# Optimization experiments

Measured on AMD Instinct MI355X. Metric: run time of the kernel, lower is better.

## Reference

```python
import jax, jax.numpy as jnp
import numpy as np

B, N, DIM, T, H, DH = 4, 2048, 512, 16, 8, 64
EPS = 1e-5


def setup_inputs() -> dict:
    key = jax.random.key(0)
    ks = jax.random.split(key, 7)
    x = jax.random.normal(ks[0], (B, N, DIM), dtype=jnp.float32)
    # time-distance matrix, e.g. months between scans, in [0, 24)
    R = jax.random.uniform(ks[1], (B, T, T), dtype=jnp.float32) * 24.0
    gamma = jnp.ones((DIM,), dtype=jnp.float32)
    beta = jnp.zeros((DIM,), dtype=jnp.float32)
    W_qkv = jax.random.normal(ks[2], (DIM, 3 * H * DH), dtype=jnp.float32) * 0.02
    W_out = jax.random.normal(ks[3], (H * DH, DIM), dtype=jnp.float32) * 0.02
    a = jax.random.uniform(ks[4], (H,), dtype=jnp.float32)          # torch.rand(heads)
    c = 12.0 * jax.random.uniform(ks[5], (H,), dtype=jnp.float32)   # 12 * torch.rand(heads)
    return {"x": x, "R": R, "gamma": gamma, "beta": beta,
            "W_qkv": W_qkv, "W_out": W_out, "a": a, "c": c}


def reference(x, R, gamma, beta, W_qkv, W_out, a, c):
    b, n, dim = x.shape
    t = R.shape[-1]
    num_patches = n // t
    scale = DH ** -0.5

    # LayerNorm
    mu = jnp.mean(x, axis=-1, keepdims=True)
    var = jnp.mean(jnp.square(x - mu), axis=-1, keepdims=True)
    xn = (x - mu) * jax.lax.rsqrt(var + EPS) * gamma + beta

    # QKV projection -> [b, h, n, d]
    qkv = xn @ W_qkv  # [b, n, 3*h*d]
    q, k, v = jnp.split(qkv, 3, axis=-1)
    def to_heads(z):
        return z.reshape(b, n, H, DH).transpose(0, 2, 1, 3)
    q, k, v = to_heads(q), to_heads(k), to_heads(v)

    # attention scores with ReLU then learned sigmoid time-decay mask
    dots = jnp.einsum('bhnd,bhmd->bhnm', q, k) * scale
    dots = jax.nn.relu(dots)

    # flipped-sigmoid decay: 1 / (1 + exp(|a|*R - |c|)), per head  -> [b, h, t, t]
    decay = 1.0 / (1.0 + jnp.exp(jnp.abs(a)[None, :, None, None] * R[:, None, :, :]
                                 - jnp.abs(c)[None, :, None, None]))
    # expand timepoint mask to token resolution (repeat_interleave on both axes)
    decay = jnp.repeat(jnp.repeat(decay, num_patches, axis=2), num_patches, axis=3)

    attn = jax.nn.softmax(dots * decay, axis=-1)
    out = jnp.einsum('bhnm,bhmd->bhnd', attn, v)
    out = out.transpose(0, 2, 1, 3).reshape(b, n, H * DH)
    return out @ W_out  # dropout is identity at eval
```

## Files before the change

### kernel.cpp

```cpp
#include <hip/hip_runtime.h>
#include <math.h>

#define B_   4
#define N_   2048
#define DIM_ 512
#define T_   16
#define H_   8
#define DH_  64

typedef unsigned short ushort_t;
typedef __attribute__((ext_vector_type(8))) short bf16x8;
typedef __attribute__((ext_vector_type(16))) float f32x16;

__device__ inline ushort_t bf16_rn(float x) {
  unsigned u = __builtin_bit_cast(unsigned, x);
  u += 0x7FFFu + ((u >> 16) & 1u);
  return (ushort_t)(u >> 16);
}
__device__ inline float bf16f(ushort_t h) {
  return __builtin_bit_cast(float, (unsigned)h << 16);
}
__device__ inline unsigned pack2(ushort_t a, ushort_t b) {
  return (unsigned)a | ((unsigned)b << 16);
}
__device__ inline void split2(float x, ushort_t &h, ushort_t &l) {
  h = bf16_rn(x);
  l = bf16_rn(x - bf16f(h));
}

__global__ __launch_bounds__(256) void transpose_split_kernel(
    const float* __restrict__ src, ushort_t* __restrict__ dh,
    ushort_t* __restrict__ dl, int K, int Nn) {
  __shared__ float Ts[64][68];
  int tid = threadIdx.x;
  int n0 = blockIdx.x * 64;
  int k0 = blockIdx.y * 64;
#pragma unroll
  for (int it = 0; it < 4; ++it) {
    int idx = tid + it * 256;
    int r = idx >> 4, c4 = (idx & 15) * 4;
    *(float4*)&Ts[r][c4] = *(const float4*)&src[(size_t)(k0 + r) * Nn + n0 + c4];
  }
  __syncthreads();
#pragma unroll
  for (int it = 0; it < 2; ++it) {
    int idx = tid + it * 256;
    int n = idx >> 3, kc = (idx & 7) * 8;
    ushort_t hs[8], ls[8];
#pragma unroll
    for (int j = 0; j < 8; ++j) split2(Ts[kc + j][n], hs[j], ls[j]);
    uint4 uh, ul;
    uh.x = pack2(hs[0], hs[1]); uh.y = pack2(hs[2], hs[3]);
    uh.z = pack2(hs[4], hs[5]); uh.w = pack2(hs[6], hs[7]);
    ul.x = pack2(ls[0], ls[1]); ul.y = pack2(ls[2], ls[3]);
    ul.z = pack2(ls[4], ls[5]); ul.w = pack2(ls[6], ls[7]);
    size_t o = (size_t)(n0 + n) * K + k0 + kc;
    *(uint4*)&dh[o] = uh;
    *(uint4*)&dl[o] = ul;
  }
}

__global__ __launch_bounds__(256) void ln_xn_kernel(
    const float* __restrict__ x, const float* __restrict__ gamma,
    const float* __restrict__ beta, ushort_t* __restrict__ xnh,
    ushort_t* __restrict__ xnl) {
  int row  = blockIdx.x * 4 + (threadIdx.x >> 6);
  int lane = threadIdx.x & 63;
  const float4* xr = (const float4*)(x + (size_t)row * DIM_);
  float4 v0 = xr[lane * 2 + 0];
  float4 v1 = xr[lane * 2 + 1];
  float s  = v0.x + v0.y + v0.z + v0.w + v1.x + v1.y + v1.z + v1.w;
  float ss = v0.x*v0.x + v0.y*v0.y + v0.z*v0.z + v0.w*v0.w
           + v1.x*v1.x + v1.y*v1.y + v1.z*v1.z + v1.w*v1.w;
#pragma unroll
  for (int off = 32; off > 0; off >>= 1) {
    s  += __shfl_xor(s, off);
    ss += __shfl_xor(ss, off);
  }
  float mu  = s * (1.0f / DIM_);
  float var = ss * (1.0f / DIM_) - mu * mu;
  float rstd = rsqrtf(var + 1e-5f);
  float4 g0 = *(const float4*)&gamma[lane * 8];
  float4 g1 = *(const float4*)&gamma[lane * 8 + 4];
  float4 b0 = *(const float4*)&beta[lane * 8];
  float4 b1 = *(const float4*)&beta[lane * 8 + 4];
  float xv[8] = {v0.x, v0.y, v0.z, v0.w, v1.x, v1.y, v1.z, v1.w};
  float gv[8] = {g0.x, g0.y, g0.z, g0.w, g1.x, g1.y, g1.z, g1.w};
  float bv[8] = {b0.x, b0.y, b0.z, b0.w, b1.x, b1.y, b1.z, b1.w};
  ushort_t hs[8], ls[8];
#pragma unroll
  for (int j = 0; j < 8; ++j) {
    float xn = (xv[j] - mu) * rstd * gv[j] + bv[j];
    split2(xn, hs[j], ls[j]);
  }
  uint4 uh, ul;
  uh.x = pack2(hs[0], hs[1]); uh.y = pack2(hs[2], hs[3]);
  uh.z = pack2(hs[4], hs[5]); uh.w = pack2(hs[6], hs[7]);
  ul.x = pack2(ls[0], ls[1]); ul.y = pack2(ls[2], ls[3]);
  ul.z = pack2(ls[4], ls[5]); ul.w = pack2(ls[6], ls[7]);
  size_t o = (size_t)row * DIM_ + lane * 8;
  *(uint4*)&xnh[o] = uh;
  *(uint4*)&xnl[o] = ul;
}

__global__ __launch_bounds__(256) void qkv_gemm_mfma(
    const ushort_t* __restrict__ xnh, const ushort_t* __restrict__ xnl,
    const ushort_t* __restrict__ wth, const ushort_t* __restrict__ wtl,
    ushort_t* __restrict__ qh, ushort_t* __restrict__ ql,
    ushort_t* __restrict__ kho, ushort_t* __restrict__ klo,
    ushort_t* __restrict__ vt) {
  __shared__ ushort_t Ah[128 * 40], Al[128 * 40], Bh[128 * 40], Bl[128 * 40];
  int tid = threadIdx.x;
  int w = tid >> 6, lane = tid & 63, l31 = lane & 31, g = lane >> 5;
  int wm = w >> 1, wn = w & 1;
  int n0 = blockIdx.x * 128;
  int m0 = blockIdx.y * 128;

  f32x16 acc[2][2];
#pragma unroll
  for (int i = 0; i < 2; ++i)
#pragma unroll
    for (int j = 0; j < 2; ++j)
#pragma unroll
      for (int e = 0; e < 16; ++e) acc[i][j][e] = 0.0f;

  int fm[2], fc[2];
#pragma unroll
  for (int it = 0; it < 2; ++it) {
    int f = tid + it * 256;
    fm[it] = f >> 2;
    fc[it] = (f & 3) * 8;
  }

#pragma unroll 1
  for (int kt = 0; kt < 16; ++kt) {
    __syncthreads();
#pragma unroll
    for (int it = 0; it < 2; ++it) {
      size_t ao = (size_t)(m0 + fm[it]) * 512 + kt * 32 + fc[it];
      size_t bo = (size_t)(n0 + fm[it]) * 512 + kt * 32 + fc[it];
      uint4 tah = *(const uint4*)&xnh[ao];
      uint4 tal = *(const uint4*)&xnl[ao];
      uint4 tbh = *(const uint4*)&wth[bo];
      uint4 tbl = *(const uint4*)&wtl[bo];
      int o = fm[it] * 40 + fc[it];
      *(uint4*)&Ah[o] = tah;
      *(uint4*)&Al[o] = tal;
      *(uint4*)&Bh[o] = tbh;
      *(uint4*)&Bl[o] = tbl;
    }
    __syncthreads();
#pragma unroll
    for (int kc = 0; kc < 2; ++kc) {
      int off = kc * 16 + 8 * g;
      bf16x8 afh[2], afl[2], bfh[2], bfl[2];
#pragma unroll
      for (int rb = 0; rb < 2; ++rb) {
        int r = (wm * 64 + rb * 32 + l31) * 40 + off;
        afh[rb] = *(const bf16x8*)&Ah[r];
        afl[rb] = *(const bf16x8*)&Al[r];
      }
#pragma unroll
      for (int cb = 0; cb < 2; ++cb) {
        int r = (wn * 64 + cb * 32 + l31) * 40 + off;
        bfh[cb] = *(const bf16x8*)&Bh[r];
        bfl[cb] = *(const bf16x8*)&Bl[r];
      }
#pragma unroll
      for (int rb = 0; rb < 2; ++rb)
#pragma unroll
        for (int cb = 0; cb < 2; ++cb) {
          acc[rb][cb] = __builtin_amdgcn_mfma_f32_32x32x16_bf16(afh[rb], bfh[cb], acc[rb][cb], 0, 0, 0);
          acc[rb][cb] = __builtin_amdgcn_mfma_f32_32x32x16_bf16(afh[rb], bfl[cb], acc[rb][cb], 0, 0, 0);
          acc[rb][cb] = __builtin_amdgcn_mfma_f32_32x32x16_bf16(afl[rb], bfh[cb], acc[rb][cb], 0, 0, 0);
        }
    }
  }

  int part = n0 >> 9;
#pragma unroll
  for (int rb = 0; rb < 2; ++rb) {
    int m_base = m0 + wm * 64 + rb * 32;
#pragma unroll
    for (int cb = 0; cb < 2; ++cb) {
      int n_g = n0 + wn * 64 + cb * 32 + l31;
      int rem = n_g & 511, hh = rem >> 6, d = rem & 63;
      if (part == 2) {
#pragma unroll
        for (int grp = 0; grp < 4; ++grp) {
          int m_g = m_base + grp * 8 + 4 * g;
          int bb = m_g >> 11, tok = m_g & 2047;
          uint2 pk;
          pk.x = pack2(bf16_rn(acc[rb][cb][grp * 4 + 0]), bf16_rn(acc[rb][cb][grp * 4 + 1]));
          pk.y = pack2(bf16_rn(acc[rb][cb][grp * 4 + 2]), bf16_rn(acc[rb][cb][grp * 4 + 3]));
          *(uint2*)&vt[((size_t)(bb * 8 + hh) * 64 + d) * 2048 + tok] = pk;
        }
      } else {
        float sc = (part == 0) ? 0.125f : 1.0f;
        ushort_t* dsth = (part == 0) ? qh : kho;
        ushort_t* dstl = (part == 0) ? ql : klo;
#pragma unroll
        for (int reg = 0; reg < 16; ++reg) {
          int row = (reg & 3) + 8 * (reg >> 2) + 4 * g;
          int m_g = m_base + row;
          int bb = m_g >> 11, tok = m_g & 2047;
          ushort_t hi, lo;
          split2(acc[rb][cb][reg] * sc, hi, lo);
          size_t addr = ((size_t)(bb * 8 + hh) * 2048 + tok) * 64 + d;
          dsth[addr] = hi;
          dstl[addr] = lo;
        }
      }
    }
  }
}

__global__ __launch_bounds__(256) void attn_mfma(
    const ushort_t* __restrict__ qh, const ushort_t* __restrict__ ql,
    const ushort_t* __restrict__ kho, const ushort_t* __restrict__ klo,
    const ushort_t* __restrict__ vt, const float* __restrict__ R,
    const float* __restrict__ a, const float* __restrict__ c,
    ushort_t* __restrict__ aoh, ushort_t* __restrict__ aol) {
  __shared__ ushort_t KhS[64 * 72], KlS[64 * 72], VtS[64 * 72], PS[64 * 72];
  __shared__ float rsLDS[2][64];

  int tid = threadIdx.x;
  int w = tid >> 6, lane = tid & 63, l31 = lane & 31, g = lane >> 5;
  int qhalf = w >> 1, khalf = w & 1;
  int bh = blockIdx.x;
  int qt = blockIdx.y;
  int b = bh >> 3, h = bh & 7;
  float aab = fabsf(a[h]);
  float cab = fabsf(c[h]);

  size_t qoff = ((size_t)bh * 2048 + qt * 64 + qhalf * 32 + l31) * 64;
  bf16x8 qfh[4], qfl[4];
#pragma unroll
  for (int d0i = 0; d0i < 4; ++d0i) {
    qfh[d0i] = *(const bf16x8*)&qh[qoff + d0i * 16 + 8 * g];
    qfl[d0i] = *(const bf16x8*)&ql[qoff + d0i * 16 + 8 * g];
  }

  int frow[2], fcc[2];
#pragma unroll
  for (int it = 0; it < 2; ++it) {
    int f = tid + it * 256;
    frow[it] = f >> 3;
    fcc[it] = (f & 7) * 8;
  }
  const ushort_t* kbase = kho + (size_t)bh * 2048 * 64;
  const ushort_t* lbase = klo + (size_t)bh * 2048 * 64;
  const ushort_t* vbase = vt + (size_t)bh * 64 * 2048;

  f32x16 oacc;
#pragma unroll
  for (int i = 0; i < 16; ++i) oacc[i] = 0.0f;
  float rs_acc[16] = {};
  int ti = qt >> 1;

#pragma unroll 1
  for (int kt = 0; kt < 32; ++kt) {
    __syncthreads();
#pragma unroll
    for (int it = 0; it < 2; ++it) {
      uint4 tk = *(const uint4*)&kbase[(size_t)(kt * 64 + frow[it]) * 64 + fcc[it]];
      uint4 tl = *(const uint4*)&lbase[(size_t)(kt * 64 + frow[it]) * 64 + fcc[it]];
      uint4 tv = *(const uint4*)&vbase[(size_t)frow[it] * 2048 + kt * 64 + fcc[it]];
      int o = frow[it] * 72 + fcc[it];
      *(uint4*)&KhS[o] = tk;
      *(uint4*)&KlS[o] = tl;
      *(uint4*)&VtS[o] = tv;
    }
    __syncthreads();

    f32x16 sacc;
#pragma unroll
    for (int i = 0; i < 16; ++i) sacc[i] = 0.0f;
    int krow = (khalf * 32 + l31) * 72;
#pragma unroll
    for (int d0i = 0; d0i < 4; ++d0i) {
      int off = krow + d0i * 16 + 8 * g;
      bf16x8 kfh = *(const bf16x8*)&KhS[off];
      bf16x8 kfl = *(const bf16x8*)&KlS[off];
      sacc = __builtin_amdgcn_mfma_f32_32x32x16_bf16(qfh[d0i], kfh, sacc, 0, 0, 0);
      sacc = __builtin_amdgcn_mfma_f32_32x32x16_bf16(qfh[d0i], kfl, sacc, 0, 0, 0);
      sacc = __builtin_amdgcn_mfma_f32_32x32x16_bf16(qfl[d0i], kfh, sacc, 0, 0, 0);
    }

    float Rv = R[b * (T_ * T_) + ti * T_ + (kt >> 1)];
    float dec = 1.0f / (1.0f + __expf(aab * Rv - cab));
#pragma unroll
    for (int reg = 0; reg < 16; ++reg) {
      float pv = __expf(fmaxf(sacc[reg], 0.0f) * dec);
      rs_acc[reg] += pv;
      int row = (reg & 3) + 8 * (reg >> 2) + 4 * g;
      PS[(qhalf * 32 + row) * 72 + khalf * 32 + l31] = bf16_rn(pv);
    }
    __syncthreads();

#pragma unroll
    for (int k0i = 0; k0i < 4; ++k0i) {
      bf16x8 pf = *(const bf16x8*)&PS[(qhalf * 32 + l31) * 72 + k0i * 16 + 8 * g];
      bf16x8 vf = *(const bf16x8*)&VtS[(khalf * 32 + l31) * 72 + k0i * 16 + 8 * g];
      oacc = __builtin_amdgcn_mfma_f32_32x32x16_bf16(pf, vf, oacc, 0, 0, 0);
    }
  }

#pragma unroll
  for (int reg = 0; reg < 16; ++reg) {
    float vsum = rs_acc[reg];
    vsum += __shfl_xor(vsum, 1);
    vsum += __shfl_xor(vsum, 2);
    vsum += __shfl_xor(vsum, 4);
    vsum += __shfl_xor(vsum, 8);
    vsum += __shfl_xor(vsum, 16);
    rs_acc[reg] = vsum;
  }
  if (l31 == 0) {
#pragma unroll
    for (int reg = 0; reg < 16; ++reg) {
      int row = (reg & 3) + 8 * (reg >> 2) + 4 * g;
      rsLDS[khalf][qhalf * 32 + row] = rs_acc[reg];
    }
  }
  __syncthreads();

#pragma unroll
  for (int reg = 0; reg < 16; ++reg) {
    int row = (reg & 3) + 8 * (reg >> 2) + 4 * g;
    int qg = qhalf * 32 + row;
    float invs = 1.0f / (rsLDS[0][qg] + rsLDS[1][qg]);
    int tok = qt * 64 + qg;
    int d = khalf * 32 + l31;
    ushort_t hi, lo;
    split2(oacc[reg] * invs, hi, lo);
    size_t addr = ((size_t)b * 2048 + tok) * 512 + h * 64 + d;
    aoh[addr] = hi;
    aol[addr] = lo;
  }
}

__global__ __launch_bounds__(256) void out_gemm_mfma(
    const ushort_t* __restrict__ ah, const ushort_t* __restrict__ al,
    const ushort_t* __restrict__ wth, const ushort_t* __restrict__ wtl,
    float* __restrict__ out) {
  __shared__ ushort_t Ah[128 * 40], Al[128 * 40], Bh[128 * 40], Bl[128 * 40];
  int tid = threadIdx.x;
  int w = tid >> 6, lane = tid & 63, l31 = lane & 31, g = lane >> 5;
  int wm = w >> 1, wn = w & 1;
  int n0 = blockIdx.x * 128;
  int m0 = blockIdx.y * 128;

  f32x16 acc[2][2];
#pragma unroll
  for (int i = 0; i < 2; ++i)
#pragma unroll
    for (int j = 0; j < 2; ++j)
#pragma unroll
      for (int e = 0; e < 16; ++e) acc[i][j][e] = 0.0f;

  int fm[2], fc[2];
#pragma unroll
  for (int it = 0; it < 2; ++it) {
    int f = tid + it * 256;
    fm[it] = f >> 2;
    fc[it] = (f & 3) * 8;
  }

#pragma unroll 1
  for (int kt = 0; kt < 16; ++kt) {
    __syncthreads();
#pragma unroll
    for (int it = 0; it < 2; ++it) {
      size_t ao = (size_t)(m0 + fm[it]) * 512 + kt * 32 + fc[it];
      size_t bo = (size_t)(n0 + fm[it]) * 512 + kt * 32 + fc[it];
      uint4 tah = *(const uint4*)&ah[ao];
      uint4 tal = *(const uint4*)&al[ao];
      uint4 tbh = *(const uint4*)&wth[bo];
      uint4 tbl = *(const uint4*)&wtl[bo];
      int o = fm[it] * 40 + fc[it];
      *(uint4*)&Ah[o] = tah;
      *(uint4*)&Al[o] = tal;
      *(uint4*)&Bh[o] = tbh;
      *(uint4*)&Bl[o] = tbl;
    }
    __syncthreads();
#pragma unroll
    for (int kc = 0; kc < 2; ++kc) {
      int off = kc * 16 + 8 * g;
      bf16x8 afh[2], afl[2], bfh[2], bfl[2];
#pragma unroll
      for (int rb = 0; rb < 2; ++rb) {
        int r = (wm * 64 + rb * 32 + l31) * 40 + off;
        afh[rb] = *(const bf16x8*)&Ah[r];
        afl[rb] = *(const bf16x8*)&Al[r];
      }
#pragma unroll
      for (int cb = 0; cb < 2; ++cb) {
        int r = (wn * 64 + cb * 32 + l31) * 40 + off;
        bfh[cb] = *(const bf16x8*)&Bh[r];
        bfl[cb] = *(const bf16x8*)&Bl[r];
      }
#pragma unroll
      for (int rb = 0; rb < 2; ++rb)
#pragma unroll
        for (int cb = 0; cb < 2; ++cb) {
          acc[rb][cb] = __builtin_amdgcn_mfma_f32_32x32x16_bf16(afh[rb], bfh[cb], acc[rb][cb], 0, 0, 0);
          acc[rb][cb] = __builtin_amdgcn_mfma_f32_32x32x16_bf16(afh[rb], bfl[cb], acc[rb][cb], 0, 0, 0);
          acc[rb][cb] = __builtin_amdgcn_mfma_f32_32x32x16_bf16(afl[rb], bfh[cb], acc[rb][cb], 0, 0, 0);
        }
    }
  }

#pragma unroll
  for (int rb = 0; rb < 2; ++rb) {
    int m_base = m0 + wm * 64 + rb * 32;
#pragma unroll
    for (int cb = 0; cb < 2; ++cb) {
      int n_g = n0 + wn * 64 + cb * 32 + l31;
#pragma unroll
      for (int reg = 0; reg < 16; ++reg) {
        int row = (reg & 3) + 8 * (reg >> 2) + 4 * g;
        out[(size_t)(m_base + row) * 512 + n_g] = acc[rb][cb][reg];
      }
    }
  }
}

extern "C" void kernel_launch(void* const* d_in, const int* in_sizes, int n_in,
                              void* d_out, int out_size, void* d_ws, size_t ws_size,
                              hipStream_t stream) {
  (void)in_sizes; (void)n_in;
  const float* x     = (const float*)d_in[0];
  const float* R     = (const float*)d_in[1];
  const float* gamma = (const float*)d_in[2];
  const float* beta  = (const float*)d_in[3];
  const float* Wqkv  = (const float*)d_in[4];
  const float* Wout  = (const float*)d_in[5];
  const float* av    = (const float*)d_in[6];
  const float* cv    = (const float*)d_in[7];
  float* out = (float*)d_out;

  const size_t EL  = (size_t)B_ * N_ * DIM_;
  const size_t SZT = EL * sizeof(ushort_t);

  char* p = (char*)d_ws;
  ushort_t* wqh = (ushort_t*)p;                  p += (size_t)1536 * 512 * 2;
  ushort_t* wql = (ushort_t*)p;                  p += (size_t)1536 * 512 * 2;
  ushort_t* woh = (ushort_t*)p;                  p += (size_t)512 * 512 * 2;
  ushort_t* wol = (ushort_t*)p;                  p += (size_t)512 * 512 * 2;
  ushort_t* qhb = (ushort_t*)p;                  p += SZT;
  ushort_t* qlb = (ushort_t*)p;                  p += SZT;
  ushort_t* khb = (ushort_t*)p;                  p += SZT;
  ushort_t* klb = (ushort_t*)p;                  p += SZT;
  ushort_t* vtb = (ushort_t*)p;                  p += SZT;
  size_t base_need = (size_t)(p - (char*)d_ws);
  size_t needA = base_need + 2 * SZT;

  bool planA = (ws_size >= needA);
  ushort_t* xnh = planA ? (ushort_t*)p : (ushort_t*)d_out;
  ushort_t* xnl = xnh + EL;
  float* gemm_dst = planA ? out : (float*)qhb;

  transpose_split_kernel<<<dim3(24, 8), dim3(256), 0, stream>>>(Wqkv, wqh, wql, 512, 1536);
  transpose_split_kernel<<<dim3(8, 8), dim3(256), 0, stream>>>(Wout, woh, wol, 512, 512);
  ln_xn_kernel<<<dim3(2048), dim3(256), 0, stream>>>(x, gamma, beta, xnh, xnl);
  qkv_gemm_mfma<<<dim3(12, 64), dim3(256), 0, stream>>>(xnh, xnl, wqh, wql,
                                                        qhb, qlb, khb, klb, vtb);
  attn_mfma<<<dim3(32, 32), dim3(256), 0, stream>>>(qhb, qlb, khb, klb, vtb,
                                                    R, av, cv, xnh, xnl);
  out_gemm_mfma<<<dim3(4, 64), dim3(256), 0, stream>>>(xnh, xnl, woh, wol, gemm_dst);
  if (!planA) {
    hipMemcpyAsync(out, gemm_dst, (size_t)out_size * sizeof(float),
                   hipMemcpyDeviceToDevice, stream);
  }
}
```

Baseline: 263.7 us.

## Merge prep kernels, add XCD-aware GEMM block mapping, use exp2 softmax

Merges the two weight transpose/split launches and the LayerNorm launch into one prep kernel that dispatches on block index, which saves launch overhead and lets the three jobs overlap. The QKV and output GEMMs switch to a 1D grid with a block-to-tile mapping that keeps the M tiles handled by the same XCD together, aiming for better L2 reuse on the MI355X's chiplets. In attention, the log2(e) factor is folded into the decay so exp2f replaces __expf, and bf16 conversion of P uses round-half-up in place of round-to-nearest-even. That rounding change alters numerics slightly.

```diff
diff --git a/kernel.cpp b/kernel.cpp
--- a/kernel.cpp
+++ b/kernel.cpp
@@ -28,79 +28,88 @@
   l = bf16_rn(x - bf16f(h));
 }
 
-__global__ __launch_bounds__(256) void transpose_split_kernel(
-    const float* __restrict__ src, ushort_t* __restrict__ dh,
-    ushort_t* __restrict__ dl, int K, int Nn) {
+__global__ __launch_bounds__(256) void prep_kernel(
+    const float* __restrict__ x, const float* __restrict__ gamma,
+    const float* __restrict__ beta, const float* __restrict__ Wqkv,
+    const float* __restrict__ Wout,
+    ushort_t* __restrict__ xnh, ushort_t* __restrict__ xnl,
+    ushort_t* __restrict__ wqh, ushort_t* __restrict__ wql,
+    ushort_t* __restrict__ woh, ushort_t* __restrict__ wol) {
   __shared__ float Ts[64][68];
+  int bidx = blockIdx.x;
   int tid = threadIdx.x;
-  int n0 = blockIdx.x * 64;
-  int k0 = blockIdx.y * 64;
-#pragma unroll
-  for (int it = 0; it < 4; ++it) {
-    int idx = tid + it * 256;
-    int r = idx >> 4, c4 = (idx & 15) * 4;
-    *(float4*)&Ts[r][c4] = *(const float4*)&src[(size_t)(k0 + r) * Nn + n0 + c4];
-  }
-  __syncthreads();
-#pragma unroll
-  for (int it = 0; it < 2; ++it) {
-    int idx = tid + it * 256;
-    int n = idx >> 3, kc = (idx & 7) * 8;
+  if (bidx < 256) {
+    const float* src; ushort_t* dh; ushort_t* dl; int Nn, n0, k0;
+    if (bidx < 192) {
+      src = Wqkv; dh = wqh; dl = wql; Nn = 1536;
+      n0 = (bidx % 24) * 64; k0 = (bidx / 24) * 64;
+    } else {
+      int l = bidx - 192;
+      src = Wout; dh = woh; dl = wol; Nn = 512;
+      n0 = (l % 8) * 64; k0 = (l / 8) * 64;
+    }
+#pragma unroll
+    for (int it = 0; it < 4; ++it) {
+      int idx = tid + it * 256;
+      int r = idx >> 4, c4 = (idx & 15) * 4;
+      *(float4*)&Ts[r][c4] = *(const float4*)&src[(size_t)(k0 + r) * Nn + n0 + c4];
+    }
+    __syncthreads();
+#pragma unroll
+    for (int it = 0; it < 2; ++it) {
+      int idx = tid + it * 256;
+      int n = idx >> 3, kc = (idx & 7) * 8;
+      ushort_t hs[8], ls[8];
+#pragma unroll
+      for (int j = 0; j < 8; ++j) split2(Ts[kc + j][n], hs[j], ls[j]);
+      uint4 uh, ul;
+      uh.x = pack2(hs[0], hs[1]); uh.y = pack2(hs[2], hs[3]);
+      uh.z = pack2(hs[4], hs[5]); uh.w = pack2(hs[6], hs[7]);
+      ul.x = pack2(ls[0], ls[1]); ul.y = pack2(ls[2], ls[3]);
+      ul.z = pack2(ls[4], ls[5]); ul.w = pack2(ls[6], ls[7]);
+      size_t o = (size_t)(n0 + n) * 512 + k0 + kc;
+      *(uint4*)&dh[o] = uh;
+      *(uint4*)&dl[o] = ul;
+    }
+  } else {
+    int row  = (bidx - 256) * 4 + (tid >> 6);
+    int lane = tid & 63;
+    const float4* xr = (const float4*)(x + (size_t)row * DIM_);
+    float4 v0 = xr[lane * 2 + 0];
+    float4 v1 = xr[lane * 2 + 1];
+    float s  = v0.x + v0.y + v0.z + v0.w + v1.x + v1.y + v1.z + v1.w;
+    float ss = v0.x*v0.x + v0.y*v0.y + v0.z*v0.z + v0.w*v0.w
+             + v1.x*v1.x + v1.y*v1.y + v1.z*v1.z + v1.w*v1.w;
+#pragma unroll
+    for (int off = 32; off > 0; off >>= 1) {
+      s  += __shfl_xor(s, off);
+      ss += __shfl_xor(ss, off);
+    }
+    float mu  = s * (1.0f / DIM_);
+    float var = ss * (1.0f / DIM_) - mu * mu;
+    float rstd = rsqrtf(var + 1e-5f);
+    float4 g0 = *(const float4*)&gamma[lane * 8];
+    float4 g1 = *(const float4*)&gamma[lane * 8 + 4];
+    float4 b0 = *(const float4*)&beta[lane * 8];
+    float4 b1 = *(const float4*)&beta[lane * 8 + 4];
+    float xv[8] = {v0.x, v0.y, v0.z, v0.w, v1.x, v1.y, v1.z, v1.w};
+    float gv[8] = {g0.x, g0.y, g0.z, g0.w, g1.x, g1.y, g1.z, g1.w};
+    float bv[8] = {b0.x, b0.y, b0.z, b0.w, b1.x, b1.y, b1.z, b1.w};
     ushort_t hs[8], ls[8];
 #pragma unroll
-    for (int j = 0; j < 8; ++j) split2(Ts[kc + j][n], hs[j], ls[j]);
+    for (int j = 0; j < 8; ++j) {
+      float xn = (xv[j] - mu) * rstd * gv[j] + bv[j];
+      split2(xn, hs[j], ls[j]);
+    }
     uint4 uh, ul;
     uh.x = pack2(hs[0], hs[1]); uh.y = pack2(hs[2], hs[3]);
     uh.z = pack2(hs[4], hs[5]); uh.w = pack2(hs[6], hs[7]);
     ul.x = pack2(ls[0], ls[1]); ul.y = pack2(ls[2], ls[3]);
     ul.z = pack2(ls[4], ls[5]); ul.w = pack2(ls[6], ls[7]);
-    size_t o = (size_t)(n0 + n) * K + k0 + kc;
-    *(uint4*)&dh[o] = uh;
-    *(uint4*)&dl[o] = ul;
-  }
-}
-
-__global__ __launch_bounds__(256) void ln_xn_kernel(
-    const float* __restrict__ x, const float* __restrict__ gamma,
-    const float* __restrict__ beta, ushort_t* __restrict__ xnh,
-    ushort_t* __restrict__ xnl) {
-  int row  = blockIdx.x * 4 + (threadIdx.x >> 6);
-  int lane = threadIdx.x & 63;
-  const float4* xr = (const float4*)(x + (size_t)row * DIM_);
-  float4 v0 = xr[lane * 2 + 0];
-  float4 v1 = xr[lane * 2 + 1];
-  float s  = v0.x + v0.y + v0.z + v0.w + v1.x + v1.y + v1.z + v1.w;
-  float ss = v0.x*v0.x + v0.y*v0.y + v0.z*v0.z + v0.w*v0.w
-           + v1.x*v1.x + v1.y*v1.y + v1.z*v1.z + v1.w*v1.w;
-#pragma unroll
-  for (int off = 32; off > 0; off >>= 1) {
-    s  += __shfl_xor(s, off);
-    ss += __shfl_xor(ss, off);
-  }
-  float mu  = s * (1.0f / DIM_);
-  float var = ss * (1.0f / DIM_) - mu * mu;
-  float rstd = rsqrtf(var + 1e-5f);
-  float4 g0 = *(const float4*)&gamma[lane * 8];
-  float4 g1 = *(const float4*)&gamma[lane * 8 + 4];
-  float4 b0 = *(const float4*)&beta[lane * 8];
-  float4 b1 = *(const float4*)&beta[lane * 8 + 4];
-  float xv[8] = {v0.x, v0.y, v0.z, v0.w, v1.x, v1.y, v1.z, v1.w};
-  float gv[8] = {g0.x, g0.y, g0.z, g0.w, g1.x, g1.y, g1.z, g1.w};
-  float bv[8] = {b0.x, b0.y, b0.z, b0.w, b1.x, b1.y, b1.z, b1.w};
-  ushort_t hs[8], ls[8];
-#pragma unroll
-  for (int j = 0; j < 8; ++j) {
-    float xn = (xv[j] - mu) * rstd * gv[j] + bv[j];
-    split2(xn, hs[j], ls[j]);
-  }
-  uint4 uh, ul;
-  uh.x = pack2(hs[0], hs[1]); uh.y = pack2(hs[2], hs[3]);
-  uh.z = pack2(hs[4], hs[5]); uh.w = pack2(hs[6], hs[7]);
-  ul.x = pack2(ls[0], ls[1]); ul.y = pack2(ls[2], ls[3]);
-  ul.z = pack2(ls[4], ls[5]); ul.w = pack2(ls[6], ls[7]);
-  size_t o = (size_t)row * DIM_ + lane * 8;
-  *(uint4*)&xnh[o] = uh;
-  *(uint4*)&xnl[o] = ul;
+    size_t o = (size_t)row * DIM_ + lane * 8;
+    *(uint4*)&xnh[o] = uh;
+    *(uint4*)&xnl[o] = ul;
+  }
 }
 
 __global__ __launch_bounds__(256) void qkv_gemm_mfma(
@@ -113,8 +122,10 @@
   int tid = threadIdx.x;
   int w = tid >> 6, lane = tid & 63, l31 = lane & 31, g = lane >> 5;
   int wm = w >> 1, wn = w & 1;
-  int n0 = blockIdx.x * 128;
-  int m0 = blockIdx.y * 128;
+  int idx = blockIdx.x;
+  int xcd = idx & 7, local = idx >> 3;
+  int n0 = (local % 12) * 128;
+  int m0 = ((local / 12) * 8 + xcd) * 128;
 
   f32x16 acc[2][2];
 #pragma unroll
@@ -288,13 +299,14 @@
     }
 
     float Rv = R[b * (T_ * T_) + ti * T_ + (kt >> 1)];
-    float dec = 1.0f / (1.0f + __expf(aab * Rv - cab));
+    float dec2 = 1.44269504f / (1.0f + __expf(aab * Rv - cab));
 #pragma unroll
     for (int reg = 0; reg < 16; ++reg) {
-      float pv = __expf(fmaxf(sacc[reg], 0.0f) * dec);
+      float pv = exp2f(fmaxf(sacc[reg], 0.0f) * dec2);
       rs_acc[reg] += pv;
       int row = (reg & 3) + 8 * (reg >> 2) + 4 * g;
-      PS[(qhalf * 32 + row) * 72 + khalf * 32 + l31] = bf16_rn(pv);
+      unsigned u = __builtin_bit_cast(unsigned, pv);
+      PS[(qhalf * 32 + row) * 72 + khalf * 32 + l31] = (ushort_t)((u + 0x8000u) >> 16);
     }
     __syncthreads();
 
@@ -348,8 +360,10 @@
   int tid = threadIdx.x;
   int w = tid >> 6, lane = tid & 63, l31 = lane & 31, g = lane >> 5;
   int wm = w >> 1, wn = w & 1;
-  int n0 = blockIdx.x * 128;
-  int m0 = blockIdx.y * 128;
+  int idx = blockIdx.x;
+  int xcd = idx & 7, local = idx >> 3;
+  int n0 = (local & 3) * 128;
+  int m0 = ((local >> 2) * 8 + xcd) * 128;
 
   f32x16 acc[2][2];
 #pragma unroll
@@ -462,14 +476,13 @@
   ushort_t* xnl = xnh + EL;
   float* gemm_dst = planA ? out : (float*)qhb;
 
-  transpose_split_kernel<<<dim3(24, 8), dim3(256), 0, stream>>>(Wqkv, wqh, wql, 512, 1536);
-  transpose_split_kernel<<<dim3(8, 8), dim3(256), 0, stream>>>(Wout, woh, wol, 512, 512);
-  ln_xn_kernel<<<dim3(2048), dim3(256), 0, stream>>>(x, gamma, beta, xnh, xnl);
-  qkv_gemm_mfma<<<dim3(12, 64), dim3(256), 0, stream>>>(xnh, xnl, wqh, wql,
-                                                        qhb, qlb, khb, klb, vtb);
+  prep_kernel<<<dim3(2304), dim3(256), 0, stream>>>(x, gamma, beta, Wqkv, Wout,
+                                                    xnh, xnl, wqh, wql, woh, wol);
+  qkv_gemm_mfma<<<dim3(768), dim3(256), 0, stream>>>(xnh, xnl, wqh, wql,
+                                                     qhb, qlb, khb, klb, vtb);
   attn_mfma<<<dim3(32, 32), dim3(256), 0, stream>>>(qhb, qlb, khb, klb, vtb,
                                                     R, av, cv, xnh, xnl);
-  out_gemm_mfma<<<dim3(4, 64), dim3(256), 0, stream>>>(xnh, xnl, woh, wol, gemm_dst);
+  out_gemm_mfma<<<dim3(256), dim3(256), 0, stream>>>(xnh, xnl, woh, wol, gemm_dst);
   if (!planA) {
     hipMemcpyAsync(out, gemm_dst, (size_t)out_size * sizeof(float),
                    hipMemcpyDeviceToDevice, stream);
```

Result: no change. 267.8 us (+1.6%).
